# Kernel optimization log

Hardware: AMD Instinct MI355X
Metric: run time of the kernel (lower is better)

## Reference

```python
import jax, jax.numpy as jnp
import numpy as np

SPARSE_SHAPE = (41, 1600, 1408)  # (D, H, W), batch_size = 1
N_VOXELS = 200000
BN_EPS = 1e-3


def _kernel_offsets():
    # 27 offsets of a 3x3x3 kernel, padding=1 -> offsets in {-1,0,1}^3
    g = np.stack(np.meshgrid(*([np.arange(-1, 2)] * 3), indexing='ij'), axis=-1)
    return jnp.asarray(g.reshape(-1, 3), dtype=jnp.int32)  # (27, 3)


def _neighbor_map(coords):
    """Submanifold rulebook: for each active voxel and each of 27 offsets,
    index of the active neighbor voxel, or N (sentinel) if inactive/out-of-bounds."""
    D, H, W = SPARSE_SHAPE
    N = coords.shape[0]
    b, z, y, x = coords[:, 0], coords[:, 1], coords[:, 2], coords[:, 3]
    flat = ((b * D + z) * H + y) * W + x  # batch_size=1
    grid = jnp.full((D * H * W,), N, dtype=jnp.int32).at[flat].set(
        jnp.arange(N, dtype=jnp.int32))
    offs = _kernel_offsets()                      # (27, 3)
    nc = coords[:, None, 1:4] + offs[None]        # (N, 27, 3)
    lim = jnp.asarray([D, H, W], dtype=jnp.int32)
    valid = jnp.all((nc >= 0) & (nc < lim), axis=-1)  # (N, 27)
    nflat = ((b[:, None] * D + nc[..., 0]) * H + nc[..., 1]) * W + nc[..., 2]
    nbr = jnp.where(valid, grid[jnp.where(valid, nflat, 0)], N)
    return nbr  # (N, 27) int32, sentinel = N


def _subm_conv(features, nbr, w):
    # gather -> batched small GEMM -> (implicit) scatter back to same voxels
    pad = jnp.concatenate(
        [features, jnp.zeros((1, features.shape[1]), features.dtype)], axis=0)
    gathered = pad[nbr]                           # (N, 27, Cin)
    return jnp.einsum('nkc,kcd->nd', gathered, w)  # (N, Cout)


def _bn_relu(x, gamma, beta):
    # BatchNorm1d in train mode over the voxel (batch) dim, eps=1e-3
    mean = x.mean(axis=0)
    var = x.var(axis=0)
    return jax.nn.relu((x - mean) * jax.lax.rsqrt(var + BN_EPS) * gamma + beta)


def setup_inputs() -> dict:
    D, H, W = SPARSE_SHAPE
    total = D * H * W
    rng = np.random.default_rng(0)
    # unique active voxel locations
    flat = np.unique(rng.integers(0, total, size=N_VOXELS + 20000))
    rng.shuffle(flat)
    flat = flat[:N_VOXELS]
    assert flat.shape[0] == N_VOXELS
    z = flat // (H * W)
    y = (flat // W) % H
    x = flat % W
    b = np.zeros_like(z)
    coords = jnp.asarray(np.stack([b, z, y, x], axis=1), dtype=jnp.int32)

    key = jax.random.key(0)
    k0, k1, k2 = jax.random.split(key, 3)
    features = jax.random.uniform(k0, (N_VOXELS, 3), dtype=jnp.float32)
    w1 = jax.random.normal(k1, (27, 3, 16), dtype=jnp.float32) * 0.1
    w2 = jax.random.normal(k2, (27, 16, 16), dtype=jnp.float32) * 0.05
    return {
        'features': features, 'coords': coords,
        'w1': w1, 'gamma1': jnp.ones(16, jnp.float32), 'beta1': jnp.zeros(16, jnp.float32),
        'w2': w2, 'gamma2': jnp.ones(16, jnp.float32), 'beta2': jnp.zeros(16, jnp.float32),
    }


def reference(features, coords, w1, gamma1, beta1, w2, gamma2, beta2):
    nbr = _neighbor_map(coords)   # shared indice_key='subm1' -> reused by both convs
    h = _bn_relu(_subm_conv(features, nbr, w1), gamma1, beta1)
    h = _bn_relu(_subm_conv(h, nbr, w2), gamma2, beta2)
    return h
```

## Files before the change

kernel.cpp:

```cpp
#include <hip/hip_runtime.h>
#include <stdint.h>

#define SPARSE_D 41
#define SPARSE_H 1600
#define SPARSE_W 1408
#define BN_EPS 0.001f

static constexpr int NYB = SPARSE_H / 2;
static constexpr int NBUCKET = SPARSE_D * NYB;
static constexpr int BCAP = 32;
static constexpr int PCAP = 12;


__global__ void k_zero(int* __restrict__ p, int n) {
    int i = blockIdx.x * blockDim.x + threadIdx.x;
    if (i < n) p[i] = 0;
}

__global__ void k_insert(const int* __restrict__ coords, int* __restrict__ bcnt,
                         uint32_t* __restrict__ bent, int N) {
    int n = blockIdx.x * blockDim.x + threadIdx.x;
    if (n >= N) return;
    int4 c4 = ((const int4*)coords)[n];
    int z = c4.y, y = c4.z, x = c4.w;
    int b = z * NYB + (y >> 1);
    int slot = atomicAdd(&bcnt[b], 1);
    if (slot < BCAP)
        bent[b * BCAP + slot] = ((uint32_t)(y & 1) << 29) | ((uint32_t)x << 18) | (uint32_t)n;
}

__device__ __forceinline__ void stats_epilogue(const float acc[16],
                                               float* __restrict__ partials,
                                               float (*sred)[32]) {
    int lid = threadIdx.x & 63;
    int wid = threadIdx.x >> 6;
    #pragma unroll
    for (int d = 0; d < 16; ++d) {
        float v = acc[d];
        float v2 = v * v;
        #pragma unroll
        for (int off = 32; off; off >>= 1) {
            v += __shfl_xor(v, off);
            v2 += __shfl_xor(v2, off);
        }
        if (lid == 0) { sred[wid][d] = v; sred[wid][16 + d] = v2; }
    }
    __syncthreads();
    if (threadIdx.x < 32) {
        float t = sred[0][threadIdx.x] + sred[1][threadIdx.x] +
                  sred[2][threadIdx.x] + sred[3][threadIdx.x];
        partials[(size_t)blockIdx.x * 32 + threadIdx.x] = t;
    }
}

__global__ void k_build_conv1(const int* __restrict__ coords, const int* __restrict__ bcnt,
                              const uint32_t* __restrict__ bent, const float* __restrict__ feat,
                              const float* __restrict__ w1,
                              int* __restrict__ pcnt, uint32_t* __restrict__ pairs,
                              float* __restrict__ h1, float* __restrict__ partials, int N) {
    __shared__ float ws[27 * 48];
    __shared__ float sred[4][32];
    for (int i = threadIdx.x; i < 27 * 48; i += blockDim.x) ws[i] = w1[i];
    __syncthreads();
    int n = blockIdx.x * blockDim.x + threadIdx.x;
    float acc[16];
    #pragma unroll
    for (int d = 0; d < 16; ++d) acc[d] = 0.f;
    if (n < N) {
        int4 c4 = ((const int4*)coords)[n];
        int z = c4.y, y = c4.z, x = c4.w;
        uint32_t lpairs[PCAP];
        int cnt = 0;
        int yb0 = (y - 1) >> 1;
        #pragma unroll
        for (int dz = -1; dz <= 1; ++dz) {
            int zz = z + dz;
            if ((unsigned)zz >= SPARSE_D) continue;
            #pragma unroll
            for (int t = 0; t < 2; ++t) {
                int yb = yb0 + t;
                if ((unsigned)yb >= NYB) continue;
                int b = zz * NYB + yb;
                int m = min(bcnt[b], BCAP);
                const uint4* p4 = (const uint4*)&bent[b * BCAP];
                for (int i = 0; i < m; i += 4) {
                    uint4 e4 = p4[i >> 2];
                    uint32_t es[4] = {e4.x, e4.y, e4.z, e4.w};
                    #pragma unroll
                    for (int j = 0; j < 4; ++j) {
                        if (i + j >= m) break;
                        uint32_t e = es[j];
                        int ey = yb * 2 + (int)(e >> 29);
                        int ex = (int)((e >> 18) & 0x7FFu);
                        int dy = ey - y, dx = ex - x;
                        if (dy < -1 || dy > 1 || dx < -1 || dx > 1) continue;
                        if (dz == 0 && dy == 0 && dx == 0) continue;
                        int k = (dz + 1) * 9 + (dy + 1) * 3 + (dx + 1);
                        if (cnt < PCAP)
                            lpairs[cnt] = ((uint32_t)k << 18) | (e & 0x3FFFFu);
                        ++cnt;
                    }
                }
            }
        }
        cnt = min(cnt, PCAP);
        pcnt[n] = cnt;
        float f0 = feat[n * 3 + 0], f1 = feat[n * 3 + 1], f2 = feat[n * 3 + 2];
        const float* w = &ws[13 * 48];
        #pragma unroll
        for (int d = 0; d < 16; ++d)
            acc[d] = fmaf(f0, w[d], fmaf(f1, w[16 + d], f2 * w[32 + d]));
        for (int c = 0; c < cnt; ++c) {
            uint32_t pr = lpairs[c];
            pairs[(size_t)c * N + n] = pr;
            int k = (int)(pr >> 18), idx = (int)(pr & 0x3FFFFu);
            float g0 = feat[idx * 3 + 0], g1 = feat[idx * 3 + 1], g2 = feat[idx * 3 + 2];
            const float* wk = &ws[k * 48];
            #pragma unroll
            for (int d = 0; d < 16; ++d)
                acc[d] = fmaf(g0, wk[d], fmaf(g1, wk[16 + d], fmaf(g2, wk[32 + d], acc[d])));
        }
        float4* o = (float4*)&h1[(size_t)n * 16];
        o[0] = make_float4(acc[0], acc[1], acc[2], acc[3]);
        o[1] = make_float4(acc[4], acc[5], acc[6], acc[7]);
        o[2] = make_float4(acc[8], acc[9], acc[10], acc[11]);
        o[3] = make_float4(acc[12], acc[13], acc[14], acc[15]);
    }
    stats_epilogue(acc, partials, sred);
}

__global__ void k_conv2(const float* __restrict__ h1, const int* __restrict__ pcnt,
                        const uint32_t* __restrict__ pairs, const float* __restrict__ w2,
                        const float* __restrict__ scsh1, float* __restrict__ out,
                        float* __restrict__ partials, int N) {
    __shared__ float ws[27 * 256];
    __shared__ float sred[4][32];
    __shared__ float sc[16], sh[16];
    for (int i = threadIdx.x; i < 27 * 256; i += blockDim.x) ws[i] = w2[i];
    if (threadIdx.x < 16) { sc[threadIdx.x] = scsh1[threadIdx.x]; sh[threadIdx.x] = scsh1[16 + threadIdx.x]; }
    __syncthreads();
    int n = blockIdx.x * blockDim.x + threadIdx.x;
    float acc[16];
    #pragma unroll
    for (int d = 0; d < 16; ++d) acc[d] = 0.f;
    if (n < N) {
        float g[16];
        #pragma unroll
        for (int c = 0; c < 16; c += 4) {
            float4 t = *(const float4*)&h1[(size_t)n * 16 + c];
            g[c]     = fmaxf(fmaf(t.x, sc[c],     sh[c]),     0.f);
            g[c + 1] = fmaxf(fmaf(t.y, sc[c + 1], sh[c + 1]), 0.f);
            g[c + 2] = fmaxf(fmaf(t.z, sc[c + 2], sh[c + 2]), 0.f);
            g[c + 3] = fmaxf(fmaf(t.w, sc[c + 3], sh[c + 3]), 0.f);
        }
        {
            const float* w = &ws[13 * 256];
            #pragma unroll
            for (int c = 0; c < 16; ++c)
                #pragma unroll
                for (int d = 0; d < 16; ++d)
                    acc[d] = fmaf(g[c], w[c * 16 + d], acc[d]);
        }
        int m = min(pcnt[n], PCAP);
        for (int cc = 0; cc < m; ++cc) {
            uint32_t pr = pairs[(size_t)cc * N + n];
            int k = (int)(pr >> 18), idx = (int)(pr & 0x3FFFFu);
            #pragma unroll
            for (int c = 0; c < 16; c += 4) {
                float4 t = *(const float4*)&h1[(size_t)idx * 16 + c];
                g[c]     = fmaxf(fmaf(t.x, sc[c],     sh[c]),     0.f);
                g[c + 1] = fmaxf(fmaf(t.y, sc[c + 1], sh[c + 1]), 0.f);
                g[c + 2] = fmaxf(fmaf(t.z, sc[c + 2], sh[c + 2]), 0.f);
                g[c + 3] = fmaxf(fmaf(t.w, sc[c + 3], sh[c + 3]), 0.f);
            }
            const float* wk = &ws[k * 256];
            #pragma unroll
            for (int c = 0; c < 16; ++c)
                #pragma unroll
                for (int d = 0; d < 16; ++d)
                    acc[d] = fmaf(g[c], wk[c * 16 + d], acc[d]);
        }
        float4* o = (float4*)&out[(size_t)n * 16];
        o[0] = make_float4(acc[0], acc[1], acc[2], acc[3]);
        o[1] = make_float4(acc[4], acc[5], acc[6], acc[7]);
        o[2] = make_float4(acc[8], acc[9], acc[10], acc[11]);
        o[3] = make_float4(acc[12], acc[13], acc[14], acc[15]);
    }
    stats_epilogue(acc, partials, sred);
}

__global__ void k_finalize(const float* __restrict__ partials, int nb,
                           const float* __restrict__ gamma, const float* __restrict__ beta,
                           float* __restrict__ scsh, float invN) {
    __shared__ float red[32][33];
    int ch = threadIdx.x & 31;
    int rg = threadIdx.x >> 5;
    float s0 = 0.f, s1 = 0.f, s2 = 0.f, s3 = 0.f;
    int j = rg;
    for (; j + 96 < nb; j += 128) {
        s0 += partials[(size_t)(j      ) * 32 + ch];
        s1 += partials[(size_t)(j + 32 ) * 32 + ch];
        s2 += partials[(size_t)(j + 64 ) * 32 + ch];
        s3 += partials[(size_t)(j + 96 ) * 32 + ch];
    }
    for (; j < nb; j += 32) s0 += partials[(size_t)j * 32 + ch];
    red[rg][ch] = (s0 + s1) + (s2 + s3);
    __syncthreads();
    if (threadIdx.x < 32) {
        float t = 0.f;
        #pragma unroll
        for (int r = 0; r < 32; ++r) t += red[r][threadIdx.x];
        red[0][threadIdx.x] = t;
    }
    __syncthreads();
    if (threadIdx.x < 16) {
        int d = threadIdx.x;
        float mean = red[0][d] * invN;
        float var = red[0][16 + d] * invN - mean * mean;
        float s2c = gamma[d] * rsqrtf(var + BN_EPS);
        scsh[d] = s2c;
        scsh[16 + d] = beta[d] - mean * s2c;
    }
}

__global__ void k_bnrelu4(float* __restrict__ x, const float* __restrict__ scsh, int nvec) {
    __shared__ float sc[16], sh[16];
    if (threadIdx.x < 16) { sc[threadIdx.x] = scsh[threadIdx.x]; sh[threadIdx.x] = scsh[16 + threadIdx.x]; }
    __syncthreads();
    int i = blockIdx.x * blockDim.x + threadIdx.x;
    if (i < nvec) {
        float4 v = ((float4*)x)[i];
        int c0 = (i & 3) * 4;
        v.x = fmaxf(fmaf(v.x, sc[c0 + 0], sh[c0 + 0]), 0.f);
        v.y = fmaxf(fmaf(v.y, sc[c0 + 1], sh[c0 + 1]), 0.f);
        v.z = fmaxf(fmaf(v.z, sc[c0 + 2], sh[c0 + 2]), 0.f);
        v.w = fmaxf(fmaf(v.w, sc[c0 + 3], sh[c0 + 3]), 0.f);
        ((float4*)x)[i] = v;
    }
}

extern "C" void kernel_launch(void* const* d_in, const int* in_sizes, int n_in,
                              void* d_out, int out_size, void* d_ws, size_t ws_size,
                              hipStream_t stream) {
    const float* feat   = (const float*)d_in[0];
    const int*   coords = (const int*)d_in[1];
    const float* w1     = (const float*)d_in[2];
    const float* gamma1 = (const float*)d_in[3];
    const float* beta1  = (const float*)d_in[4];
    const float* w2     = (const float*)d_in[5];
    const float* gamma2 = (const float*)d_in[6];
    const float* beta2  = (const float*)d_in[7];
    float* out = (float*)d_out;
    const int N = in_sizes[0] / 3;

    const int T = 256;
    const int nb = (N + T - 1) / T;
    const int nvec = N * 16 / 4;
    const int nbv = (nvec + T - 1) / T;

    char* ws = (char*)d_ws;
    size_t off = 0;
    int* bcnt = (int*)(ws + off);            off += ((size_t)NBUCKET * 4 + 63) & ~(size_t)63;
    uint32_t* bent = (uint32_t*)(ws + off);  off += (size_t)NBUCKET * BCAP * 4;
    int* pcnt = (int*)(ws + off);            off += ((size_t)N * 4 + 63) & ~(size_t)63;
    uint32_t* pairs = (uint32_t*)(ws + off); off += (size_t)PCAP * N * 4;
    float* h1 = (float*)(ws + off);          off += (size_t)N * 16 * 4;
    float* partials = (float*)(ws + off);    off += ((size_t)nb * 32 * 4 + 63) & ~(size_t)63;
    float* stats = (float*)(ws + off);

    k_zero<<<(NBUCKET + T - 1) / T, T, 0, stream>>>(bcnt, NBUCKET);
    k_insert<<<nb, T, 0, stream>>>(coords, bcnt, bent, N);
    k_build_conv1<<<nb, T, 0, stream>>>(coords, bcnt, bent, feat, w1, pcnt, pairs, h1, partials, N);
    k_finalize<<<1, 1024, 0, stream>>>(partials, nb, gamma1, beta1, stats, 1.f / (float)N);
    k_conv2<<<nb, T, 0, stream>>>(h1, pcnt, pairs, w2, stats, out, partials, N);
    k_finalize<<<1, 1024, 0, stream>>>(partials, nb, gamma2, beta2, stats + 32, 1.f / (float)N);
    k_bnrelu4<<<nbv, T, 0, stream>>>(out, stats + 32, nvec);
}
```

Baseline: 158.5 us.

## Fuse all stages into one persistent kernel with grid-wide barriers

Replaces the seven separate launches (zero, insert, build+conv1, finalize, conv2, finalize, bnrelu) with one persistent kernel of 256 blocks that uses a software grid barrier between phases. The bucket count is stored in slot 0 of each bucket line and the scan is fully unrolled over two uint4 groups, and BN statistics are accumulated per thread across a grid-stride loop before one reduction. The aim is to remove launch gaps and tail effects between the small kernels. In exchange it relies on all 256 blocks being co-resident for the spin barrier, and occupancy may be lower because both weight tables now sit in shared memory at once.

New measurement: 511.0 us. 222% more time.

```diff
diff --git a/kernel.cpp b/kernel.cpp
--- a/kernel.cpp
+++ b/kernel.cpp
@@ -8,36 +8,37 @@
 
 static constexpr int NYB = SPARSE_H / 2;
 static constexpr int NBUCKET = SPARSE_D * NYB;
-static constexpr int BCAP = 32;
 static constexpr int PCAP = 12;
-
-
-__global__ void k_zero(int* __restrict__ p, int n) {
-    int i = blockIdx.x * blockDim.x + threadIdx.x;
-    if (i < n) p[i] = 0;
-}
-
-__global__ void k_insert(const int* __restrict__ coords, int* __restrict__ bcnt,
-                         uint32_t* __restrict__ bent, int N) {
-    int n = blockIdx.x * blockDim.x + threadIdx.x;
-    if (n >= N) return;
-    int4 c4 = ((const int4*)coords)[n];
-    int z = c4.y, y = c4.z, x = c4.w;
-    int b = z * NYB + (y >> 1);
-    int slot = atomicAdd(&bcnt[b], 1);
-    if (slot < BCAP)
-        bent[b * BCAP + slot] = ((uint32_t)(y & 1) << 29) | ((uint32_t)x << 18) | (uint32_t)n;
-}
-
-__device__ __forceinline__ void stats_epilogue(const float acc[16],
-                                               float* __restrict__ partials,
-                                               float (*sred)[32]) {
+static constexpr int GRIDB = 256;
+static constexpr int BLOCKT = 256;
+static constexpr int GSZ = GRIDB * BLOCKT;
+
+
+__device__ __forceinline__ void gbar(int* __restrict__ counter, int* __restrict__ gen) {
+    __syncthreads();
+    if (threadIdx.x == 0) {
+        __threadfence();
+        int g = __hip_atomic_load(gen, __ATOMIC_RELAXED, __HIP_MEMORY_SCOPE_AGENT);
+        if (__hip_atomic_fetch_add(counter, 1, __ATOMIC_ACQ_REL, __HIP_MEMORY_SCOPE_AGENT) == GRIDB - 1) {
+            __hip_atomic_store(counter, 0, __ATOMIC_RELAXED, __HIP_MEMORY_SCOPE_AGENT);
+            __hip_atomic_fetch_add(gen, 1, __ATOMIC_ACQ_REL, __HIP_MEMORY_SCOPE_AGENT);
+        } else {
+            while (__hip_atomic_load(gen, __ATOMIC_ACQUIRE, __HIP_MEMORY_SCOPE_AGENT) == g)
+                __builtin_amdgcn_s_sleep(2);
+        }
+        __threadfence();
+    }
+    __syncthreads();
+}
+
+__device__ __forceinline__ void stats_epilogue2(const float s[16], const float q[16],
+                                                float* __restrict__ partials,
+                                                float (*sred)[32]) {
     int lid = threadIdx.x & 63;
     int wid = threadIdx.x >> 6;
     #pragma unroll
     for (int d = 0; d < 16; ++d) {
-        float v = acc[d];
-        float v2 = v * v;
+        float v = s[d], v2 = q[d];
         #pragma unroll
         for (int off = 32; off; off >>= 1) {
             v += __shfl_xor(v, off);
@@ -46,196 +47,260 @@
         if (lid == 0) { sred[wid][d] = v; sred[wid][16 + d] = v2; }
     }
     __syncthreads();
-    if (threadIdx.x < 32) {
-        float t = sred[0][threadIdx.x] + sred[1][threadIdx.x] +
-                  sred[2][threadIdx.x] + sred[3][threadIdx.x];
-        partials[(size_t)blockIdx.x * 32 + threadIdx.x] = t;
-    }
-}
-
-__global__ void k_build_conv1(const int* __restrict__ coords, const int* __restrict__ bcnt,
-                              const uint32_t* __restrict__ bent, const float* __restrict__ feat,
-                              const float* __restrict__ w1,
-                              int* __restrict__ pcnt, uint32_t* __restrict__ pairs,
-                              float* __restrict__ h1, float* __restrict__ partials, int N) {
-    __shared__ float ws[27 * 48];
-    __shared__ float sred[4][32];
-    for (int i = threadIdx.x; i < 27 * 48; i += blockDim.x) ws[i] = w1[i];
-    __syncthreads();
-    int n = blockIdx.x * blockDim.x + threadIdx.x;
-    float acc[16];
-    #pragma unroll
-    for (int d = 0; d < 16; ++d) acc[d] = 0.f;
-    if (n < N) {
-        int4 c4 = ((const int4*)coords)[n];
-        int z = c4.y, y = c4.z, x = c4.w;
-        uint32_t lpairs[PCAP];
-        int cnt = 0;
-        int yb0 = (y - 1) >> 1;
-        #pragma unroll
-        for (int dz = -1; dz <= 1; ++dz) {
-            int zz = z + dz;
-            if ((unsigned)zz >= SPARSE_D) continue;
-            #pragma unroll
-            for (int t = 0; t < 2; ++t) {
-                int yb = yb0 + t;
-                if ((unsigned)yb >= NYB) continue;
-                int b = zz * NYB + yb;
-                int m = min(bcnt[b], BCAP);
-                const uint4* p4 = (const uint4*)&bent[b * BCAP];
-                for (int i = 0; i < m; i += 4) {
-                    uint4 e4 = p4[i >> 2];
-                    uint32_t es[4] = {e4.x, e4.y, e4.z, e4.w};
-                    #pragma unroll
-                    for (int j = 0; j < 4; ++j) {
-                        if (i + j >= m) break;
-                        uint32_t e = es[j];
-                        int ey = yb * 2 + (int)(e >> 29);
-                        int ex = (int)((e >> 18) & 0x7FFu);
-                        int dy = ey - y, dx = ex - x;
-                        if (dy < -1 || dy > 1 || dx < -1 || dx > 1) continue;
-                        if (dz == 0 && dy == 0 && dx == 0) continue;
-                        int k = (dz + 1) * 9 + (dy + 1) * 3 + (dx + 1);
-                        if (cnt < PCAP)
-                            lpairs[cnt] = ((uint32_t)k << 18) | (e & 0x3FFFFu);
-                        ++cnt;
-                    }
-                }
-            }
-        }
-        cnt = min(cnt, PCAP);
-        pcnt[n] = cnt;
-        float f0 = feat[n * 3 + 0], f1 = feat[n * 3 + 1], f2 = feat[n * 3 + 2];
-        const float* w = &ws[13 * 48];
-        #pragma unroll
-        for (int d = 0; d < 16; ++d)
-            acc[d] = fmaf(f0, w[d], fmaf(f1, w[16 + d], f2 * w[32 + d]));
-        for (int c = 0; c < cnt; ++c) {
-            uint32_t pr = lpairs[c];
-            pairs[(size_t)c * N + n] = pr;
-            int k = (int)(pr >> 18), idx = (int)(pr & 0x3FFFFu);
-            float g0 = feat[idx * 3 + 0], g1 = feat[idx * 3 + 1], g2 = feat[idx * 3 + 2];
-            const float* wk = &ws[k * 48];
-            #pragma unroll
-            for (int d = 0; d < 16; ++d)
-                acc[d] = fmaf(g0, wk[d], fmaf(g1, wk[16 + d], fmaf(g2, wk[32 + d], acc[d])));
-        }
-        float4* o = (float4*)&h1[(size_t)n * 16];
-        o[0] = make_float4(acc[0], acc[1], acc[2], acc[3]);
-        o[1] = make_float4(acc[4], acc[5], acc[6], acc[7]);
-        o[2] = make_float4(acc[8], acc[9], acc[10], acc[11]);
-        o[3] = make_float4(acc[12], acc[13], acc[14], acc[15]);
-    }
-    stats_epilogue(acc, partials, sred);
-}
-
-__global__ void k_conv2(const float* __restrict__ h1, const int* __restrict__ pcnt,
-                        const uint32_t* __restrict__ pairs, const float* __restrict__ w2,
-                        const float* __restrict__ scsh1, float* __restrict__ out,
-                        float* __restrict__ partials, int N) {
-    __shared__ float ws[27 * 256];
-    __shared__ float sred[4][32];
-    __shared__ float sc[16], sh[16];
-    for (int i = threadIdx.x; i < 27 * 256; i += blockDim.x) ws[i] = w2[i];
-    if (threadIdx.x < 16) { sc[threadIdx.x] = scsh1[threadIdx.x]; sh[threadIdx.x] = scsh1[16 + threadIdx.x]; }
-    __syncthreads();
-    int n = blockIdx.x * blockDim.x + threadIdx.x;
-    float acc[16];
-    #pragma unroll
-    for (int d = 0; d < 16; ++d) acc[d] = 0.f;
-    if (n < N) {
-        float g[16];
-        #pragma unroll
-        for (int c = 0; c < 16; c += 4) {
-            float4 t = *(const float4*)&h1[(size_t)n * 16 + c];
-            g[c]     = fmaxf(fmaf(t.x, sc[c],     sh[c]),     0.f);
-            g[c + 1] = fmaxf(fmaf(t.y, sc[c + 1], sh[c + 1]), 0.f);
-            g[c + 2] = fmaxf(fmaf(t.z, sc[c + 2], sh[c + 2]), 0.f);
-            g[c + 3] = fmaxf(fmaf(t.w, sc[c + 3], sh[c + 3]), 0.f);
-        }
-        {
-            const float* w = &ws[13 * 256];
-            #pragma unroll
-            for (int c = 0; c < 16; ++c)
-                #pragma unroll
-                for (int d = 0; d < 16; ++d)
-                    acc[d] = fmaf(g[c], w[c * 16 + d], acc[d]);
-        }
-        int m = min(pcnt[n], PCAP);
-        for (int cc = 0; cc < m; ++cc) {
-            uint32_t pr = pairs[(size_t)cc * N + n];
-            int k = (int)(pr >> 18), idx = (int)(pr & 0x3FFFFu);
-            #pragma unroll
-            for (int c = 0; c < 16; c += 4) {
-                float4 t = *(const float4*)&h1[(size_t)idx * 16 + c];
-                g[c]     = fmaxf(fmaf(t.x, sc[c],     sh[c]),     0.f);
-                g[c + 1] = fmaxf(fmaf(t.y, sc[c + 1], sh[c + 1]), 0.f);
-                g[c + 2] = fmaxf(fmaf(t.z, sc[c + 2], sh[c + 2]), 0.f);
-                g[c + 3] = fmaxf(fmaf(t.w, sc[c + 3], sh[c + 3]), 0.f);
-            }
-            const float* wk = &ws[k * 256];
-            #pragma unroll
-            for (int c = 0; c < 16; ++c)
-                #pragma unroll
-                for (int d = 0; d < 16; ++d)
-                    acc[d] = fmaf(g[c], wk[c * 16 + d], acc[d]);
-        }
-        float4* o = (float4*)&out[(size_t)n * 16];
-        o[0] = make_float4(acc[0], acc[1], acc[2], acc[3]);
-        o[1] = make_float4(acc[4], acc[5], acc[6], acc[7]);
-        o[2] = make_float4(acc[8], acc[9], acc[10], acc[11]);
-        o[3] = make_float4(acc[12], acc[13], acc[14], acc[15]);
-    }
-    stats_epilogue(acc, partials, sred);
-}
-
-__global__ void k_finalize(const float* __restrict__ partials, int nb,
-                           const float* __restrict__ gamma, const float* __restrict__ beta,
-                           float* __restrict__ scsh, float invN) {
-    __shared__ float red[32][33];
+    if (threadIdx.x < 32)
+        partials[(size_t)blockIdx.x * 32 + threadIdx.x] =
+            sred[0][threadIdx.x] + sred[1][threadIdx.x] +
+            sred[2][threadIdx.x] + sred[3][threadIdx.x];
+    __syncthreads();
+}
+
+__device__ __forceinline__ void reduce_scsh(const float* __restrict__ partials,
+                                            const float* __restrict__ gamma,
+                                            const float* __restrict__ beta,
+                                            float invN, float (*red)[33],
+                                            float* __restrict__ scsh) {
     int ch = threadIdx.x & 31;
     int rg = threadIdx.x >> 5;
     float s0 = 0.f, s1 = 0.f, s2 = 0.f, s3 = 0.f;
-    int j = rg;
-    for (; j + 96 < nb; j += 128) {
-        s0 += partials[(size_t)(j      ) * 32 + ch];
-        s1 += partials[(size_t)(j + 32 ) * 32 + ch];
-        s2 += partials[(size_t)(j + 64 ) * 32 + ch];
-        s3 += partials[(size_t)(j + 96 ) * 32 + ch];
-    }
-    for (; j < nb; j += 32) s0 += partials[(size_t)j * 32 + ch];
+    #pragma unroll
+    for (int j = 0; j < GRIDB / 32; ++j) {
+        int base = rg + j * 32;
+        s0 += partials[(size_t)(base     ) * 32 + ch];
+        s1 += partials[(size_t)(base +  8) * 32 + ch];
+        s2 += partials[(size_t)(base + 16) * 32 + ch];
+        s3 += partials[(size_t)(base + 24) * 32 + ch];
+    }
     red[rg][ch] = (s0 + s1) + (s2 + s3);
     __syncthreads();
     if (threadIdx.x < 32) {
         float t = 0.f;
         #pragma unroll
-        for (int r = 0; r < 32; ++r) t += red[r][threadIdx.x];
+        for (int r = 0; r < 8; ++r) t += red[r][threadIdx.x];
         red[0][threadIdx.x] = t;
     }
     __syncthreads();
     if (threadIdx.x < 16) {
         int d = threadIdx.x;
         float mean = red[0][d] * invN;
-        float var = red[0][16 + d] * invN - mean * mean;
-        float s2c = gamma[d] * rsqrtf(var + BN_EPS);
-        scsh[d] = s2c;
-        scsh[16 + d] = beta[d] - mean * s2c;
-    }
-}
-
-__global__ void k_bnrelu4(float* __restrict__ x, const float* __restrict__ scsh, int nvec) {
-    __shared__ float sc[16], sh[16];
-    if (threadIdx.x < 16) { sc[threadIdx.x] = scsh[threadIdx.x]; sh[threadIdx.x] = scsh[16 + threadIdx.x]; }
-    __syncthreads();
-    int i = blockIdx.x * blockDim.x + threadIdx.x;
-    if (i < nvec) {
-        float4 v = ((float4*)x)[i];
-        int c0 = (i & 3) * 4;
-        v.x = fmaxf(fmaf(v.x, sc[c0 + 0], sh[c0 + 0]), 0.f);
-        v.y = fmaxf(fmaf(v.y, sc[c0 + 1], sh[c0 + 1]), 0.f);
-        v.z = fmaxf(fmaf(v.z, sc[c0 + 2], sh[c0 + 2]), 0.f);
-        v.w = fmaxf(fmaf(v.w, sc[c0 + 3], sh[c0 + 3]), 0.f);
-        ((float4*)x)[i] = v;
+        float var  = red[0][16 + d] * invN - mean * mean;
+        float sc = gamma[d] * rsqrtf(var + BN_EPS);
+        scsh[d] = sc;
+        scsh[16 + d] = beta[d] - mean * sc;
+    }
+    __syncthreads();
+}
+
+__global__ void k_mega(const int* __restrict__ coords, const float* __restrict__ feat,
+                       const float* __restrict__ w1, const float* __restrict__ gamma1,
+                       const float* __restrict__ beta1, const float* __restrict__ w2,
+                       const float* __restrict__ gamma2, const float* __restrict__ beta2,
+                       uint32_t* __restrict__ bent, uint32_t* __restrict__ pairs,
+                       int* __restrict__ pcnt, float* __restrict__ partials1,
+                       float* __restrict__ partials2, float* __restrict__ h1,
+                       float* __restrict__ out, int* __restrict__ bar, int N) {
+    __shared__ float w1s[27 * 48];
+    __shared__ float w2s[27 * 256];
+    __shared__ float red[8][33];
+    __shared__ float sred[4][32];
+    __shared__ float scsh[32];
+
+    for (int i = threadIdx.x; i < 27 * 48; i += BLOCKT) w1s[i] = w1[i];
+    for (int i = threadIdx.x; i < 27 * 256; i += BLOCKT) w2s[i] = w2[i];
+
+    int* bcounter = bar;
+    int* bgen = bar + 1;
+    const int gtid = blockIdx.x * BLOCKT + threadIdx.x;
+    const float invN = 1.f / (float)N;
+
+    for (int b = gtid; b < NBUCKET; b += GSZ) bent[(size_t)b * 32] = 0u;
+    gbar(bcounter, bgen);
+
+    for (int n = gtid; n < N; n += GSZ) {
+        int4 c4 = ((const int4*)coords)[n];
+        int z = c4.y, y = c4.z, x = c4.w;
+        int b = z * NYB + (y >> 1);
+        uint32_t e = ((uint32_t)(y & 1) << 29) | ((uint32_t)x << 18) | (uint32_t)n;
+        int slot = atomicAdd((int*)&bent[(size_t)b * 32], 1) + 1;
+        if (slot <= 31) bent[(size_t)b * 32 + slot] = e;
+    }
+    gbar(bcounter, bgen);
+
+    {
+        float sum1[16], sq1[16];
+        #pragma unroll
+        for (int d = 0; d < 16; ++d) { sum1[d] = 0.f; sq1[d] = 0.f; }
+        for (int n = gtid; n < N; n += GSZ) {
+            int4 c4 = ((const int4*)coords)[n];
+            int z = c4.y, y = c4.z, x = c4.w;
+            float acc[16];
+            {
+                float f0 = feat[n * 3 + 0], f1 = feat[n * 3 + 1], f2 = feat[n * 3 + 2];
+                const float* wd = &w1s[13 * 48];
+                #pragma unroll
+                for (int d = 0; d < 16; ++d)
+                    acc[d] = fmaf(f0, wd[d], fmaf(f1, wd[16 + d], f2 * wd[32 + d]));
+            }
+            int cnt = 0;
+            auto scan_entry = [&](uint32_t e, int slot, int m, int yb, int dzk) {
+                if (slot > m) return;
+                int ey = (yb << 1) + (int)(e >> 29);
+                int ex = (int)((e >> 18) & 0x7FFu);
+                int dy = ey - y, dx = ex - x;
+                if ((unsigned)(dy + 1) > 2u || (unsigned)(dx + 1) > 2u) return;
+                uint32_t idx = e & 0x3FFFFu;
+                if (idx == (uint32_t)n) return;
+                int k = dzk + (dy + 1) * 3 + (dx + 1);
+                if (cnt < PCAP) pairs[(size_t)cnt * N + n] = ((uint32_t)k << 18) | idx;
+                ++cnt;
+                float g0 = feat[idx * 3 + 0], g1 = feat[idx * 3 + 1], g2 = feat[idx * 3 + 2];
+                const float* wk = &w1s[k * 48];
+                #pragma unroll
+                for (int d = 0; d < 16; ++d)
+                    acc[d] = fmaf(g0, wk[d], fmaf(g1, wk[16 + d], fmaf(g2, wk[32 + d], acc[d])));
+            };
+            int yb0 = (y - 1) >> 1;
+            #pragma unroll
+            for (int dz = -1; dz <= 1; ++dz) {
+                int zz = z + dz;
+                if ((unsigned)zz >= SPARSE_D) continue;
+                int dzk = (dz + 1) * 9;
+                #pragma unroll
+                for (int t = 0; t < 2; ++t) {
+                    int yb = yb0 + t;
+                    if ((unsigned)yb >= NYB) continue;
+                    const uint4* L = (const uint4*)&bent[((size_t)zz * NYB + yb) * 32];
+                    uint4 q0 = L[0], q1 = L[1], q2 = L[2], q3 = L[3];
+                    int m = min((int)q0.x, 31);
+                    scan_entry(q0.y,  1, m, yb, dzk);
+                    scan_entry(q0.z,  2, m, yb, dzk);
+                    scan_entry(q0.w,  3, m, yb, dzk);
+                    scan_entry(q1.x,  4, m, yb, dzk);
+                    scan_entry(q1.y,  5, m, yb, dzk);
+                    scan_entry(q1.z,  6, m, yb, dzk);
+                    scan_entry(q1.w,  7, m, yb, dzk);
+                    scan_entry(q2.x,  8, m, yb, dzk);
+                    scan_entry(q2.y,  9, m, yb, dzk);
+                    scan_entry(q2.z, 10, m, yb, dzk);
+                    scan_entry(q2.w, 11, m, yb, dzk);
+                    scan_entry(q3.x, 12, m, yb, dzk);
+                    scan_entry(q3.y, 13, m, yb, dzk);
+                    scan_entry(q3.z, 14, m, yb, dzk);
+                    scan_entry(q3.w, 15, m, yb, dzk);
+                    if (m > 15) {
+                        uint4 q4 = L[4], q5 = L[5], q6 = L[6], q7 = L[7];
+                        scan_entry(q4.x, 16, m, yb, dzk);
+                        scan_entry(q4.y, 17, m, yb, dzk);
+                        scan_entry(q4.z, 18, m, yb, dzk);
+                        scan_entry(q4.w, 19, m, yb, dzk);
+                        scan_entry(q5.x, 20, m, yb, dzk);
+                        scan_entry(q5.y, 21, m, yb, dzk);
+                        scan_entry(q5.z, 22, m, yb, dzk);
+                        scan_entry(q5.w, 23, m, yb, dzk);
+                        scan_entry(q6.x, 24, m, yb, dzk);
+                        scan_entry(q6.y, 25, m, yb, dzk);
+                        scan_entry(q6.z, 26, m, yb, dzk);
+                        scan_entry(q6.w, 27, m, yb, dzk);
+                        scan_entry(q7.x, 28, m, yb, dzk);
+                        scan_entry(q7.y, 29, m, yb, dzk);
+                        scan_entry(q7.z, 30, m, yb, dzk);
+                        scan_entry(q7.w, 31, m, yb, dzk);
+                    }
+                }
+            }
+            pcnt[n] = min(cnt, PCAP);
+            float4* o = (float4*)&h1[(size_t)n * 16];
+            o[0] = make_float4(acc[0], acc[1], acc[2], acc[3]);
+            o[1] = make_float4(acc[4], acc[5], acc[6], acc[7]);
+            o[2] = make_float4(acc[8], acc[9], acc[10], acc[11]);
+            o[3] = make_float4(acc[12], acc[13], acc[14], acc[15]);
+            #pragma unroll
+            for (int d = 0; d < 16; ++d) {
+                sum1[d] += acc[d];
+                sq1[d] = fmaf(acc[d], acc[d], sq1[d]);
+            }
+        }
+        stats_epilogue2(sum1, sq1, partials1, sred);
+    }
+    gbar(bcounter, bgen);
+
+    reduce_scsh(partials1, gamma1, beta1, invN, red, scsh);
+    {
+        float sum2[16], sq2[16];
+        #pragma unroll
+        for (int d = 0; d < 16; ++d) { sum2[d] = 0.f; sq2[d] = 0.f; }
+        for (int n = gtid; n < N; n += GSZ) {
+            float a2[16];
+            #pragma unroll
+            for (int d = 0; d < 16; ++d) a2[d] = 0.f;
+            {
+                const float4* hp = (const float4*)&h1[(size_t)n * 16];
+                const float* wk = &w2s[13 * 256];
+                #pragma unroll
+                for (int cb = 0; cb < 4; ++cb) {
+                    float4 tq = hp[cb];
+                    float g0 = fmaxf(fmaf(tq.x, scsh[cb * 4 + 0], scsh[16 + cb * 4 + 0]), 0.f);
+                    float g1 = fmaxf(fmaf(tq.y, scsh[cb * 4 + 1], scsh[16 + cb * 4 + 1]), 0.f);
+                    float g2 = fmaxf(fmaf(tq.z, scsh[cb * 4 + 2], scsh[16 + cb * 4 + 2]), 0.f);
+                    float g3 = fmaxf(fmaf(tq.w, scsh[cb * 4 + 3], scsh[16 + cb * 4 + 3]), 0.f);
+                    #pragma unroll
+                    for (int d = 0; d < 16; ++d) {
+                        a2[d] = fmaf(g0, wk[(cb * 4 + 0) * 16 + d], a2[d]);
+                        a2[d] = fmaf(g1, wk[(cb * 4 + 1) * 16 + d], a2[d]);
+                        a2[d] = fmaf(g2, wk[(cb * 4 + 2) * 16 + d], a2[d]);
+                        a2[d] = fmaf(g3, wk[(cb * 4 + 3) * 16 + d], a2[d]);
+                    }
+                }
+            }
+            int m = pcnt[n];
+            for (int cc = 0; cc < m; ++cc) {
+                uint32_t pr = pairs[(size_t)cc * N + n];
+                int k = (int)(pr >> 18);
+                int idx = (int)(pr & 0x3FFFFu);
+                const float* wk = &w2s[k * 256];
+                const float4* hp = (const float4*)&h1[(size_t)idx * 16];
+                #pragma unroll
+                for (int cb = 0; cb < 4; ++cb) {
+                    float4 tq = hp[cb];
+                    float g0 = fmaxf(fmaf(tq.x, scsh[cb * 4 + 0], scsh[16 + cb * 4 + 0]), 0.f);
+                    float g1 = fmaxf(fmaf(tq.y, scsh[cb * 4 + 1], scsh[16 + cb * 4 + 1]), 0.f);
+                    float g2 = fmaxf(fmaf(tq.z, scsh[cb * 4 + 2], scsh[16 + cb * 4 + 2]), 0.f);
+                    float g3 = fmaxf(fmaf(tq.w, scsh[cb * 4 + 3], scsh[16 + cb * 4 + 3]), 0.f);
+                    #pragma unroll
+                    for (int d = 0; d < 16; ++d) {
+                        a2[d] = fmaf(g0, wk[(cb * 4 + 0) * 16 + d], a2[d]);
+                        a2[d] = fmaf(g1, wk[(cb * 4 + 1) * 16 + d], a2[d]);
+                        a2[d] = fmaf(g2, wk[(cb * 4 + 2) * 16 + d], a2[d]);
+                        a2[d] = fmaf(g3, wk[(cb * 4 + 3) * 16 + d], a2[d]);
+                    }
+                }
+            }
+            float4* o = (float4*)&out[(size_t)n * 16];
+            o[0] = make_float4(a2[0], a2[1], a2[2], a2[3]);
+            o[1] = make_float4(a2[4], a2[5], a2[6], a2[7]);
+            o[2] = make_float4(a2[8], a2[9], a2[10], a2[11]);
+            o[3] = make_float4(a2[12], a2[13], a2[14], a2[15]);
+            #pragma unroll
+            for (int d = 0; d < 16; ++d) {
+                sum2[d] += a2[d];
+                sq2[d] = fmaf(a2[d], a2[d], sq2[d]);
+            }
+        }
+        stats_epilogue2(sum2, sq2, partials2, sred);
+    }
+    gbar(bcounter, bgen);
+
+    reduce_scsh(partials2, gamma2, beta2, invN, red, scsh);
+    {
+        const int nvec = N * 4;
+        for (int i = gtid; i < nvec; i += GSZ) {
+            float4 v = ((float4*)out)[i];
+            int c0 = (i & 3) * 4;
+            v.x = fmaxf(fmaf(v.x, scsh[c0 + 0], scsh[16 + c0 + 0]), 0.f);
+            v.y = fmaxf(fmaf(v.y, scsh[c0 + 1], scsh[16 + c0 + 1]), 0.f);
+            v.z = fmaxf(fmaf(v.z, scsh[c0 + 2], scsh[16 + c0 + 2]), 0.f);
+            v.w = fmaxf(fmaf(v.w, scsh[c0 + 3], scsh[16 + c0 + 3]), 0.f);
+            ((float4*)out)[i] = v;
+        }
     }
 }
 
@@ -253,26 +318,18 @@
     float* out = (float*)d_out;
     const int N = in_sizes[0] / 3;
 
-    const int T = 256;
-    const int nb = (N + T - 1) / T;
-    const int nvec = N * 16 / 4;
-    const int nbv = (nvec + T - 1) / T;
-
     char* ws = (char*)d_ws;
     size_t off = 0;
-    int* bcnt = (int*)(ws + off);            off += ((size_t)NBUCKET * 4 + 63) & ~(size_t)63;
-    uint32_t* bent = (uint32_t*)(ws + off);  off += (size_t)NBUCKET * BCAP * 4;
+    int* bar = (int*)(ws + off);             off += 64;
+    uint32_t* bent = (uint32_t*)(ws + off);  off += (size_t)NBUCKET * 32 * 4;
+    uint32_t* pairs = (uint32_t*)(ws + off); off += (size_t)PCAP * N * 4;
     int* pcnt = (int*)(ws + off);            off += ((size_t)N * 4 + 63) & ~(size_t)63;
-    uint32_t* pairs = (uint32_t*)(ws + off); off += (size_t)PCAP * N * 4;
+    float* partials1 = (float*)(ws + off);   off += (size_t)GRIDB * 32 * 4;
+    float* partials2 = (float*)(ws + off);   off += (size_t)GRIDB * 32 * 4;
     float* h1 = (float*)(ws + off);          off += (size_t)N * 16 * 4;
-    float* partials = (float*)(ws + off);    off += ((size_t)nb * 32 * 4 + 63) & ~(size_t)63;
-    float* stats = (float*)(ws + off);
-
-    k_zero<<<(NBUCKET + T - 1) / T, T, 0, stream>>>(bcnt, NBUCKET);
-    k_insert<<<nb, T, 0, stream>>>(coords, bcnt, bent, N);
-    k_build_conv1<<<nb, T, 0, stream>>>(coords, bcnt, bent, feat, w1, pcnt, pairs, h1, partials, N);
-    k_finalize<<<1, 1024, 0, stream>>>(partials, nb, gamma1, beta1, stats, 1.f / (float)N);
-    k_conv2<<<nb, T, 0, stream>>>(h1, pcnt, pairs, w2, stats, out, partials, N);
-    k_finalize<<<1, 1024, 0, stream>>>(partials, nb, gamma2, beta2, stats + 32, 1.f / (float)N);
-    k_bnrelu4<<<nbv, T, 0, stream>>>(out, stats + 32, nvec);
-}
+
+    hipMemsetAsync(bar, 0, 64, stream);
+    k_mega<<<GRIDB, BLOCKT, 0, stream>>>(coords, feat, w1, gamma1, beta1,
+                                         w2, gamma2, beta2, bent, pairs, pcnt,
+                                         partials1, partials2, h1, out, bar, N);
+}
```

## Fold BN stat finalization into consumer kernels and drop finalize launches

Applied to the files above, without the earlier changes.

Removes the two single-block finalize kernels. Each block of conv2 and of the final BN-ReLU kernel now reduces the roughly 782 partial-sum rows itself to compute scale and shift, and the final BN-ReLU becomes a grid-stride loop. The bucket zeroing kernel is replaced with hipMemsetAsync, and the neighbor self-check compares indices with unsigned range tests. This cuts two serialized single-block launches at the cost of redundant partial reductions in every block (about 100KB read per block).

New measurement: 166.2 us. 1.05x slower.

```diff
diff --git a/kernel.cpp b/kernel.cpp
--- a/kernel.cpp
+++ b/kernel.cpp
@@ -11,11 +11,6 @@
 static constexpr int BCAP = 32;
 static constexpr int PCAP = 12;
 
-
-__global__ void k_zero(int* __restrict__ p, int n) {
-    int i = blockIdx.x * blockDim.x + threadIdx.x;
-    if (i < n) p[i] = 0;
-}
 
 __global__ void k_insert(const int* __restrict__ coords, int* __restrict__ bcnt,
                          uint32_t* __restrict__ bent, int N) {
@@ -46,11 +41,46 @@
         if (lid == 0) { sred[wid][d] = v; sred[wid][16 + d] = v2; }
     }
     __syncthreads();
+    if (threadIdx.x < 32)
+        partials[(size_t)blockIdx.x * 32 + threadIdx.x] =
+            sred[0][threadIdx.x] + sred[1][threadIdx.x] +
+            sred[2][threadIdx.x] + sred[3][threadIdx.x];
+}
+
+__device__ __forceinline__ void reduce_scsh(const float* __restrict__ partials, int nbp,
+                                            const float* __restrict__ gamma,
+                                            const float* __restrict__ beta,
+                                            float invN, float (*red)[33],
+                                            float* __restrict__ scsh) {
+    int ch = threadIdx.x & 31;
+    int rg = threadIdx.x >> 5;
+    float s0 = 0.f, s1 = 0.f, s2 = 0.f, s3 = 0.f;
+    int j = rg;
+    for (; j + 24 < nbp; j += 32) {
+        s0 += partials[(size_t)(j     ) * 32 + ch];
+        s1 += partials[(size_t)(j +  8) * 32 + ch];
+        s2 += partials[(size_t)(j + 16) * 32 + ch];
+        s3 += partials[(size_t)(j + 24) * 32 + ch];
+    }
+    for (; j < nbp; j += 8) s0 += partials[(size_t)j * 32 + ch];
+    red[rg][ch] = (s0 + s1) + (s2 + s3);
+    __syncthreads();
     if (threadIdx.x < 32) {
-        float t = sred[0][threadIdx.x] + sred[1][threadIdx.x] +
-                  sred[2][threadIdx.x] + sred[3][threadIdx.x];
-        partials[(size_t)blockIdx.x * 32 + threadIdx.x] = t;
-    }
+        float t = 0.f;
+        #pragma unroll
+        for (int r = 0; r < 8; ++r) t += red[r][threadIdx.x];
+        red[0][threadIdx.x] = t;
+    }
+    __syncthreads();
+    if (threadIdx.x < 16) {
+        int d = threadIdx.x;
+        float mean = red[0][d] * invN;
+        float var  = red[0][16 + d] * invN - mean * mean;
+        float sc = gamma[d] * rsqrtf(var + BN_EPS);
+        scsh[d] = sc;
+        scsh[16 + d] = beta[d] - mean * sc;
+    }
+    __syncthreads();
 }
 
 __global__ void k_build_conv1(const int* __restrict__ coords, const int* __restrict__ bcnt,
@@ -90,14 +120,15 @@
                     for (int j = 0; j < 4; ++j) {
                         if (i + j >= m) break;
                         uint32_t e = es[j];
-                        int ey = yb * 2 + (int)(e >> 29);
+                        int ey = (yb << 1) + (int)(e >> 29);
                         int ex = (int)((e >> 18) & 0x7FFu);
                         int dy = ey - y, dx = ex - x;
-                        if (dy < -1 || dy > 1 || dx < -1 || dx > 1) continue;
-                        if (dz == 0 && dy == 0 && dx == 0) continue;
+                        if ((unsigned)(dy + 1) > 2u || (unsigned)(dx + 1) > 2u) continue;
+                        uint32_t idx = e & 0x3FFFFu;
+                        if (idx == (uint32_t)n) continue;
                         int k = (dz + 1) * 9 + (dy + 1) * 3 + (dx + 1);
                         if (cnt < PCAP)
-                            lpairs[cnt] = ((uint32_t)k << 18) | (e & 0x3FFFFu);
+                            lpairs[cnt] = ((uint32_t)k << 18) | idx;
                         ++cnt;
                     }
                 }
@@ -131,14 +162,16 @@
 
 __global__ void k_conv2(const float* __restrict__ h1, const int* __restrict__ pcnt,
                         const uint32_t* __restrict__ pairs, const float* __restrict__ w2,
-                        const float* __restrict__ scsh1, float* __restrict__ out,
-                        float* __restrict__ partials, int N) {
+                        const float* __restrict__ partials1, int nbp,
+                        const float* __restrict__ gamma1, const float* __restrict__ beta1,
+                        float invN, float* __restrict__ out,
+                        float* __restrict__ partials2, int N) {
     __shared__ float ws[27 * 256];
+    __shared__ float red[8][33];
     __shared__ float sred[4][32];
-    __shared__ float sc[16], sh[16];
+    __shared__ float scsh[32];
     for (int i = threadIdx.x; i < 27 * 256; i += blockDim.x) ws[i] = w2[i];
-    if (threadIdx.x < 16) { sc[threadIdx.x] = scsh1[threadIdx.x]; sh[threadIdx.x] = scsh1[16 + threadIdx.x]; }
-    __syncthreads();
+    reduce_scsh(partials1, nbp, gamma1, beta1, invN, red, scsh);
     int n = blockIdx.x * blockDim.x + threadIdx.x;
     float acc[16];
     #pragma unroll
@@ -148,10 +181,10 @@
         #pragma unroll
         for (int c = 0; c < 16; c += 4) {
             float4 t = *(const float4*)&h1[(size_t)n * 16 + c];
-            g[c]     = fmaxf(fmaf(t.x, sc[c],     sh[c]),     0.f);
-            g[c + 1] = fmaxf(fmaf(t.y, sc[c + 1], sh[c + 1]), 0.f);
-            g[c + 2] = fmaxf(fmaf(t.z, sc[c + 2], sh[c + 2]), 0.f);
-            g[c + 3] = fmaxf(fmaf(t.w, sc[c + 3], sh[c + 3]), 0.f);
+            g[c]     = fmaxf(fmaf(t.x, scsh[c],     scsh[16 + c]),     0.f);
+            g[c + 1] = fmaxf(fmaf(t.y, scsh[c + 1], scsh[16 + c + 1]), 0.f);
+            g[c + 2] = fmaxf(fmaf(t.z, scsh[c + 2], scsh[16 + c + 2]), 0.f);
+            g[c + 3] = fmaxf(fmaf(t.w, scsh[c + 3], scsh[16 + c + 3]), 0.f);
         }
         {
             const float* w = &ws[13 * 256];
@@ -168,10 +201,10 @@
             #pragma unroll
             for (int c = 0; c < 16; c += 4) {
                 float4 t = *(const float4*)&h1[(size_t)idx * 16 + c];
-                g[c]     = fmaxf(fmaf(t.x, sc[c],     sh[c]),     0.f);
-                g[c + 1] = fmaxf(fmaf(t.y, sc[c + 1], sh[c + 1]), 0.f);
-                g[c + 2] = fmaxf(fmaf(t.z, sc[c + 2], sh[c + 2]), 0.f);
-                g[c + 3] = fmaxf(fmaf(t.w, sc[c + 3], sh[c + 3]), 0.f);
+                g[c]     = fmaxf(fmaf(t.x, scsh[c],     scsh[16 + c]),     0.f);
+                g[c + 1] = fmaxf(fmaf(t.y, scsh[c + 1], scsh[16 + c + 1]), 0.f);
+                g[c + 2] = fmaxf(fmaf(t.z, scsh[c + 2], scsh[16 + c + 2]), 0.f);
+                g[c + 3] = fmaxf(fmaf(t.w, scsh[c + 3], scsh[16 + c + 3]), 0.f);
             }
             const float* wk = &ws[k * 256];
             #pragma unroll
@@ -186,56 +219,24 @@
         o[2] = make_float4(acc[8], acc[9], acc[10], acc[11]);
         o[3] = make_float4(acc[12], acc[13], acc[14], acc[15]);
     }
-    stats_epilogue(acc, partials, sred);
-}
-
-__global__ void k_finalize(const float* __restrict__ partials, int nb,
-                           const float* __restrict__ gamma, const float* __restrict__ beta,
-                           float* __restrict__ scsh, float invN) {
-    __shared__ float red[32][33];
-    int ch = threadIdx.x & 31;
-    int rg = threadIdx.x >> 5;
-    float s0 = 0.f, s1 = 0.f, s2 = 0.f, s3 = 0.f;
-    int j = rg;
-    for (; j + 96 < nb; j += 128) {
-        s0 += partials[(size_t)(j      ) * 32 + ch];
-        s1 += partials[(size_t)(j + 32 ) * 32 + ch];
-        s2 += partials[(size_t)(j + 64 ) * 32 + ch];
-        s3 += partials[(size_t)(j + 96 ) * 32 + ch];
-    }
-    for (; j < nb; j += 32) s0 += partials[(size_t)j * 32 + ch];
-    red[rg][ch] = (s0 + s1) + (s2 + s3);
-    __syncthreads();
-    if (threadIdx.x < 32) {
-        float t = 0.f;
-        #pragma unroll
-        for (int r = 0; r < 32; ++r) t += red[r][threadIdx.x];
-        red[0][threadIdx.x] = t;
-    }
-    __syncthreads();
-    if (threadIdx.x < 16) {
-        int d = threadIdx.x;
-        float mean = red[0][d] * invN;
-        float var = red[0][16 + d] * invN - mean * mean;
-        float s2c = gamma[d] * rsqrtf(var + BN_EPS);
-        scsh[d] = s2c;
-        scsh[16 + d] = beta[d] - mean * s2c;
-    }
-}
-
-__global__ void k_bnrelu4(float* __restrict__ x, const float* __restrict__ scsh, int nvec) {
-    __shared__ float sc[16], sh[16];
-    if (threadIdx.x < 16) { sc[threadIdx.x] = scsh[threadIdx.x]; sh[threadIdx.x] = scsh[16 + threadIdx.x]; }
-    __syncthreads();
-    int i = blockIdx.x * blockDim.x + threadIdx.x;
-    if (i < nvec) {
-        float4 v = ((float4*)x)[i];
+    stats_epilogue(acc, partials2, sred);
+}
+
+__global__ void k_bnrelu(float* __restrict__ out, const float* __restrict__ partials2,
+                         int nbp, const float* __restrict__ gamma2,
+                         const float* __restrict__ beta2, float invN, int nvec) {
+    __shared__ float red[8][33];
+    __shared__ float scsh[32];
+    reduce_scsh(partials2, nbp, gamma2, beta2, invN, red, scsh);
+    int stride = gridDim.x * blockDim.x;
+    for (int i = blockIdx.x * blockDim.x + threadIdx.x; i < nvec; i += stride) {
+        float4 v = ((float4*)out)[i];
         int c0 = (i & 3) * 4;
-        v.x = fmaxf(fmaf(v.x, sc[c0 + 0], sh[c0 + 0]), 0.f);
-        v.y = fmaxf(fmaf(v.y, sc[c0 + 1], sh[c0 + 1]), 0.f);
-        v.z = fmaxf(fmaf(v.z, sc[c0 + 2], sh[c0 + 2]), 0.f);
-        v.w = fmaxf(fmaf(v.w, sc[c0 + 3], sh[c0 + 3]), 0.f);
-        ((float4*)x)[i] = v;
+        v.x = fmaxf(fmaf(v.x, scsh[c0 + 0], scsh[16 + c0 + 0]), 0.f);
+        v.y = fmaxf(fmaf(v.y, scsh[c0 + 1], scsh[16 + c0 + 1]), 0.f);
+        v.z = fmaxf(fmaf(v.z, scsh[c0 + 2], scsh[16 + c0 + 2]), 0.f);
+        v.w = fmaxf(fmaf(v.w, scsh[c0 + 3], scsh[16 + c0 + 3]), 0.f);
+        ((float4*)out)[i] = v;
     }
 }
 
@@ -256,7 +257,7 @@
     const int T = 256;
     const int nb = (N + T - 1) / T;
     const int nvec = N * 16 / 4;
-    const int nbv = (nvec + T - 1) / T;
+    const float invN = 1.f / (float)N;
 
     char* ws = (char*)d_ws;
     size_t off = 0;
@@ -265,14 +266,13 @@
     int* pcnt = (int*)(ws + off);            off += ((size_t)N * 4 + 63) & ~(size_t)63;
     uint32_t* pairs = (uint32_t*)(ws + off); off += (size_t)PCAP * N * 4;
     float* h1 = (float*)(ws + off);          off += (size_t)N * 16 * 4;
-    float* partials = (float*)(ws + off);    off += ((size_t)nb * 32 * 4 + 63) & ~(size_t)63;
-    float* stats = (float*)(ws + off);
-
-    k_zero<<<(NBUCKET + T - 1) / T, T, 0, stream>>>(bcnt, NBUCKET);
+    float* partials1 = (float*)(ws + off);   off += ((size_t)nb * 32 * 4 + 63) & ~(size_t)63;
+    float* partials2 = (float*)(ws + off);   off += ((size_t)nb * 32 * 4 + 63) & ~(size_t)63;
+
+    hipMemsetAsync(bcnt, 0, (size_t)NBUCKET * 4, stream);
     k_insert<<<nb, T, 0, stream>>>(coords, bcnt, bent, N);
-    k_build_conv1<<<nb, T, 0, stream>>>(coords, bcnt, bent, feat, w1, pcnt, pairs, h1, partials, N);
-    k_finalize<<<1, 1024, 0, stream>>>(partials, nb, gamma1, beta1, stats, 1.f / (float)N);
-    k_conv2<<<nb, T, 0, stream>>>(h1, pcnt, pairs, w2, stats, out, partials, N);
-    k_finalize<<<1, 1024, 0, stream>>>(partials, nb, gamma2, beta2, stats + 32, 1.f / (float)N);
-    k_bnrelu4<<<nbv, T, 0, stream>>>(out, stats + 32, nvec);
-}
+    k_build_conv1<<<nb, T, 0, stream>>>(coords, bcnt, bent, feat, w1, pcnt, pairs, h1, partials1, N);
+    k_conv2<<<nb, T, 0, stream>>>(h1, pcnt, pairs, w2, partials1, nb, gamma1, beta1, invN,
+                                  out, partials2, N);
+    k_bnrelu<<<nb, T, 0, stream>>>(out, partials2, nb, gamma2, beta2, invN, nvec);
+}
```

## Embed bucket counts in hash entries and read conv weights from global memory

Applied to the files above, without the earlier changes.

Stores each bucket's count in its first slot so a single vector load yields the count and three entries, and prefetches all six neighbor buckets before scanning. This removes the separate count array and zero kernel, replacing them with a memset over the full bucket array. Weight staging into shared memory is dropped in both conv kernels in favor of cached global reads. The trade-offs are a much larger memset, one fewer slot per bucket, and possibly slower divergent weight reads.

New measurement: 154.5 us. -2.5%, faster.

```diff
diff --git a/kernel.cpp b/kernel.cpp
--- a/kernel.cpp
+++ b/kernel.cpp
@@ -8,25 +8,18 @@
 
 static constexpr int NYB = SPARSE_H / 2;
 static constexpr int NBUCKET = SPARSE_D * NYB;
-static constexpr int BCAP = 32;
 static constexpr int PCAP = 12;
 
 
-__global__ void k_zero(int* __restrict__ p, int n) {
-    int i = blockIdx.x * blockDim.x + threadIdx.x;
-    if (i < n) p[i] = 0;
-}
-
-__global__ void k_insert(const int* __restrict__ coords, int* __restrict__ bcnt,
-                         uint32_t* __restrict__ bent, int N) {
+__global__ void k_insert(const int* __restrict__ coords, uint32_t* __restrict__ bent, int N) {
     int n = blockIdx.x * blockDim.x + threadIdx.x;
     if (n >= N) return;
     int4 c4 = ((const int4*)coords)[n];
     int z = c4.y, y = c4.z, x = c4.w;
     int b = z * NYB + (y >> 1);
-    int slot = atomicAdd(&bcnt[b], 1);
-    if (slot < BCAP)
-        bent[b * BCAP + slot] = ((uint32_t)(y & 1) << 29) | ((uint32_t)x << 18) | (uint32_t)n;
+    uint32_t e = ((uint32_t)(y & 1) << 29) | ((uint32_t)x << 18) | (uint32_t)n;
+    int slot = atomicAdd((int*)&bent[(size_t)b * 32], 1) + 1;
+    if (slot <= 31) bent[(size_t)b * 32 + slot] = e;
 }
 
 __device__ __forceinline__ void stats_epilogue(const float acc[16],
@@ -46,22 +39,17 @@
         if (lid == 0) { sred[wid][d] = v; sred[wid][16 + d] = v2; }
     }
     __syncthreads();
-    if (threadIdx.x < 32) {
-        float t = sred[0][threadIdx.x] + sred[1][threadIdx.x] +
-                  sred[2][threadIdx.x] + sred[3][threadIdx.x];
-        partials[(size_t)blockIdx.x * 32 + threadIdx.x] = t;
-    }
-}
-
-__global__ void k_build_conv1(const int* __restrict__ coords, const int* __restrict__ bcnt,
-                              const uint32_t* __restrict__ bent, const float* __restrict__ feat,
-                              const float* __restrict__ w1,
+    if (threadIdx.x < 32)
+        partials[(size_t)blockIdx.x * 32 + threadIdx.x] =
+            sred[0][threadIdx.x] + sred[1][threadIdx.x] +
+            sred[2][threadIdx.x] + sred[3][threadIdx.x];
+}
+
+__global__ void k_build_conv1(const int* __restrict__ coords, const uint32_t* __restrict__ bent,
+                              const float* __restrict__ feat, const float* __restrict__ w1,
                               int* __restrict__ pcnt, uint32_t* __restrict__ pairs,
                               float* __restrict__ h1, float* __restrict__ partials, int N) {
-    __shared__ float ws[27 * 48];
     __shared__ float sred[4][32];
-    for (int i = threadIdx.x; i < 27 * 48; i += blockDim.x) ws[i] = w1[i];
-    __syncthreads();
     int n = blockIdx.x * blockDim.x + threadIdx.x;
     float acc[16];
     #pragma unroll
@@ -69,53 +57,65 @@
     if (n < N) {
         int4 c4 = ((const int4*)coords)[n];
         int z = c4.y, y = c4.z, x = c4.w;
+
+        float f0 = feat[n * 3 + 0], f1 = feat[n * 3 + 1], f2 = feat[n * 3 + 2];
+        const float* wd = w1 + 13 * 48;
+        #pragma unroll
+        for (int d = 0; d < 16; ++d)
+            acc[d] = fmaf(f0, wd[d], fmaf(f1, wd[16 + d], f2 * wd[32 + d]));
+
+        int yb0 = (y - 1) >> 1;
+        uint4 q0[6];
+        int bix[6], mm[6];
+        #pragma unroll
+        for (int p = 0; p < 6; ++p) {
+            int zz = z + p / 2 - 1;
+            int yb = yb0 + (p & 1);
+            bool v = ((unsigned)zz < SPARSE_D) & ((unsigned)yb < NYB);
+            int b = v ? (zz * NYB + yb) : 0;
+            bix[p] = b;
+            q0[p] = *(const uint4*)&bent[(size_t)b * 32];
+            mm[p] = v ? 1 : 0;
+        }
+
         uint32_t lpairs[PCAP];
         int cnt = 0;
-        int yb0 = (y - 1) >> 1;
-        #pragma unroll
-        for (int dz = -1; dz <= 1; ++dz) {
-            int zz = z + dz;
-            if ((unsigned)zz >= SPARSE_D) continue;
-            #pragma unroll
-            for (int t = 0; t < 2; ++t) {
-                int yb = yb0 + t;
-                if ((unsigned)yb >= NYB) continue;
-                int b = zz * NYB + yb;
-                int m = min(bcnt[b], BCAP);
-                const uint4* p4 = (const uint4*)&bent[b * BCAP];
-                for (int i = 0; i < m; i += 4) {
-                    uint4 e4 = p4[i >> 2];
-                    uint32_t es[4] = {e4.x, e4.y, e4.z, e4.w};
-                    #pragma unroll
-                    for (int j = 0; j < 4; ++j) {
-                        if (i + j >= m) break;
-                        uint32_t e = es[j];
-                        int ey = yb * 2 + (int)(e >> 29);
-                        int ex = (int)((e >> 18) & 0x7FFu);
-                        int dy = ey - y, dx = ex - x;
-                        if (dy < -1 || dy > 1 || dx < -1 || dx > 1) continue;
-                        if (dz == 0 && dy == 0 && dx == 0) continue;
-                        int k = (dz + 1) * 9 + (dy + 1) * 3 + (dx + 1);
-                        if (cnt < PCAP)
-                            lpairs[cnt] = ((uint32_t)k << 18) | (e & 0x3FFFFu);
-                        ++cnt;
-                    }
-                }
+        #pragma unroll
+        for (int p = 0; p < 6; ++p) {
+            int m = mm[p] ? min((int)q0[p].x, 31) : 0;
+            int yb = yb0 + (p & 1);
+            int dzk = (p / 2) * 9;
+            auto scan_entry = [&](uint32_t e, int slot) {
+                if (slot > m) return;
+                int ey = (yb << 1) + (int)(e >> 29);
+                int ex = (int)((e >> 18) & 0x7FFu);
+                int dy = ey - y, dx = ex - x;
+                if ((unsigned)(dy + 1) > 2u || (unsigned)(dx + 1) > 2u) return;
+                uint32_t idx = e & 0x3FFFFu;
+                if (idx == (uint32_t)n) return;
+                int k = dzk + (dy + 1) * 3 + (dx + 1);
+                if (cnt < PCAP) lpairs[cnt] = ((uint32_t)k << 18) | idx;
+                ++cnt;
+            };
+            scan_entry(q0[p].y, 1);
+            scan_entry(q0[p].z, 2);
+            scan_entry(q0[p].w, 3);
+            for (int w = 4; w <= m; w += 4) {
+                uint4 q = *(const uint4*)&bent[(size_t)bix[p] * 32 + w];
+                scan_entry(q.x, w);
+                scan_entry(q.y, w + 1);
+                scan_entry(q.z, w + 2);
+                scan_entry(q.w, w + 3);
             }
         }
         cnt = min(cnt, PCAP);
         pcnt[n] = cnt;
-        float f0 = feat[n * 3 + 0], f1 = feat[n * 3 + 1], f2 = feat[n * 3 + 2];
-        const float* w = &ws[13 * 48];
-        #pragma unroll
-        for (int d = 0; d < 16; ++d)
-            acc[d] = fmaf(f0, w[d], fmaf(f1, w[16 + d], f2 * w[32 + d]));
         for (int c = 0; c < cnt; ++c) {
             uint32_t pr = lpairs[c];
             pairs[(size_t)c * N + n] = pr;
             int k = (int)(pr >> 18), idx = (int)(pr & 0x3FFFFu);
             float g0 = feat[idx * 3 + 0], g1 = feat[idx * 3 + 1], g2 = feat[idx * 3 + 2];
-            const float* wk = &ws[k * 48];
+            const float* wk = w1 + k * 48;
             #pragma unroll
             for (int d = 0; d < 16; ++d)
                 acc[d] = fmaf(g0, wk[d], fmaf(g1, wk[16 + d], fmaf(g2, wk[32 + d], acc[d])));
@@ -133,10 +133,8 @@
                         const uint32_t* __restrict__ pairs, const float* __restrict__ w2,
                         const float* __restrict__ scsh1, float* __restrict__ out,
                         float* __restrict__ partials, int N) {
-    __shared__ float ws[27 * 256];
     __shared__ float sred[4][32];
     __shared__ float sc[16], sh[16];
-    for (int i = threadIdx.x; i < 27 * 256; i += blockDim.x) ws[i] = w2[i];
     if (threadIdx.x < 16) { sc[threadIdx.x] = scsh1[threadIdx.x]; sh[threadIdx.x] = scsh1[16 + threadIdx.x]; }
     __syncthreads();
     int n = blockIdx.x * blockDim.x + threadIdx.x;
@@ -154,7 +152,7 @@
             g[c + 3] = fmaxf(fmaf(t.w, sc[c + 3], sh[c + 3]), 0.f);
         }
         {
-            const float* w = &ws[13 * 256];
+            const float* w = w2 + 13 * 256;
             #pragma unroll
             for (int c = 0; c < 16; ++c)
                 #pragma unroll
@@ -173,7 +171,7 @@
                 g[c + 2] = fmaxf(fmaf(t.z, sc[c + 2], sh[c + 2]), 0.f);
                 g[c + 3] = fmaxf(fmaf(t.w, sc[c + 3], sh[c + 3]), 0.f);
             }
-            const float* wk = &ws[k * 256];
+            const float* wk = w2 + k * 256;
             #pragma unroll
             for (int c = 0; c < 16; ++c)
                 #pragma unroll
@@ -260,17 +258,16 @@
 
     char* ws = (char*)d_ws;
     size_t off = 0;
-    int* bcnt = (int*)(ws + off);            off += ((size_t)NBUCKET * 4 + 63) & ~(size_t)63;
-    uint32_t* bent = (uint32_t*)(ws + off);  off += (size_t)NBUCKET * BCAP * 4;
+    uint32_t* bent = (uint32_t*)(ws + off);  off += (size_t)NBUCKET * 32 * 4;
     int* pcnt = (int*)(ws + off);            off += ((size_t)N * 4 + 63) & ~(size_t)63;
     uint32_t* pairs = (uint32_t*)(ws + off); off += (size_t)PCAP * N * 4;
     float* h1 = (float*)(ws + off);          off += (size_t)N * 16 * 4;
     float* partials = (float*)(ws + off);    off += ((size_t)nb * 32 * 4 + 63) & ~(size_t)63;
     float* stats = (float*)(ws + off);
 
-    k_zero<<<(NBUCKET + T - 1) / T, T, 0, stream>>>(bcnt, NBUCKET);
-    k_insert<<<nb, T, 0, stream>>>(coords, bcnt, bent, N);
-    k_build_conv1<<<nb, T, 0, stream>>>(coords, bcnt, bent, feat, w1, pcnt, pairs, h1, partials, N);
+    hipMemsetAsync(bent, 0, (size_t)NBUCKET * 32 * 4, stream);
+    k_insert<<<nb, T, 0, stream>>>(coords, bent, N);
+    k_build_conv1<<<nb, T, 0, stream>>>(coords, bent, feat, w1, pcnt, pairs, h1, partials, N);
     k_finalize<<<1, 1024, 0, stream>>>(partials, nb, gamma1, beta1, stats, 1.f / (float)N);
     k_conv2<<<nb, T, 0, stream>>>(h1, pcnt, pairs, w2, stats, out, partials, N);
     k_finalize<<<1, 1024, 0, stream>>>(partials, nb, gamma2, beta2, stats + 32, 1.f / (float)N);
```
